# Performance work log

Hardware: AMD Instinct MI355X
Metric: run time of the kernel (lower is better)

## Reference

```python
import jax, jax.numpy as jnp
import numpy as np

B, T, C, H = 1, 4096, 512, 8
HS = C // H  # head size = 64
ROPE_BASE = 10000.0


def setup_inputs() -> dict:
    key = jax.random.key(0)
    k1, k2, k3 = jax.random.split(key, 3)
    x = jax.random.normal(k1, (B, T, C), dtype=jnp.float32)
    W_attn = jax.random.normal(k2, (3 * C, C), dtype=jnp.float32) * 0.02
    W_proj = jax.random.normal(k3, (C, C), dtype=jnp.float32) * 0.02
    # RoPE cache: (T, HS//2, 2) = (cos, sin) per position/frequency
    pos = jnp.arange(T, dtype=jnp.float32)
    inv_freq = 1.0 / (ROPE_BASE ** (jnp.arange(0, HS, 2, dtype=jnp.float32) / HS))
    ang = pos[:, None] * inv_freq[None, :]  # (T, HS//2)
    rope = jnp.stack([jnp.cos(ang), jnp.sin(ang)], axis=-1)
    # causal mask (1,1,T,T), True = attend
    mask = jnp.tril(jnp.ones((T, T), dtype=bool))[None, None]
    return {"x": x, "rope": rope, "mask": mask, "W_attn": W_attn, "W_proj": W_proj}


def apply_rope(x, rope):
    # x: (B, T, H, hs); rope: (>=T, hs//2, 2)
    b, t, h, d = x.shape
    xs = x.reshape(b, t, h, d // 2, 2)
    rc = rope[:t].reshape(1, t, 1, d // 2, 2)
    real = xs[..., 0] * rc[..., 0] - xs[..., 1] * rc[..., 1]
    imag = xs[..., 1] * rc[..., 0] + xs[..., 0] * rc[..., 1]
    return jnp.stack([real, imag], axis=-1).reshape(b, t, h, d)


def reference(x, rope, mask, W_attn, W_proj):
    b, t, c = x.shape
    qkv = x @ W_attn.T  # (B,T,3C)
    q, k, v = jnp.split(qkv, 3, axis=2)
    q = q.reshape(b, t, H, HS)
    k = k.reshape(b, t, H, HS)
    v = v.reshape(b, t, H, HS)
    q = apply_rope(q, rope)
    k = apply_rope(k, rope)
    # (B,H,T,hs)
    q = q.transpose(0, 2, 1, 3)
    k = k.transpose(0, 2, 1, 3)
    v = v.transpose(0, 2, 1, 3)
    scores = jnp.einsum('bhqd,bhkd->bhqk', q, k) * (1.0 / np.sqrt(HS).astype(np.float32))
    scores = jnp.where(mask, scores, -jnp.inf)
    att = jax.nn.softmax(scores, axis=-1)
    y = jnp.einsum('bhqk,bhkd->bhqd', att, v)
    y = y.transpose(0, 2, 1, 3).reshape(b, t, c)
    return y @ W_proj.T
```

## Files before the change

### kernel.cpp

```cpp
#include <hip/hip_runtime.h>

#define T_ 4096
#define C_ 512
#define H_ 8
#define HS_ 64

typedef __attribute__((ext_vector_type(8))) short s16x8;
typedef __attribute__((ext_vector_type(4))) float f32x4;
typedef unsigned int u32;

__device__ __forceinline__ float bf2f(short u) {
    union { float f; unsigned int i; } v;
    v.i = ((unsigned int)(unsigned short)u) << 16;
    return v.f;
}
__device__ __forceinline__ short f2bf(float f) {
    union { float f; unsigned int i; } v;
    v.f = f;
    unsigned int r = (v.i + 0x7FFFu + ((v.i >> 16) & 1u)) >> 16;
    return (short)r;
}

__device__ __forceinline__ void gload_lds16(const short* g, short* l) {
    __builtin_amdgcn_global_load_lds((const __attribute__((address_space(1))) u32*)g,
                                     (__attribute__((address_space(3))) u32*)l,
                                     16, 0, 0);
}

__global__ void cvt3_kernel(const float* __restrict__ x, const float* __restrict__ wa,
                            const float* __restrict__ wp,
                            short* __restrict__ xb, short* __restrict__ wab,
                            short* __restrict__ wpb) {
    int b = blockIdx.x, tid = threadIdx.x;
    const float* src; short* dst; int i;
    if (b < 2048)      { src = x;  dst = xb;  i = b * 256 + tid; }
    else if (b < 2816) { src = wa; dst = wab; i = (b - 2048) * 256 + tid; }
    else               { src = wp; dst = wpb; i = (b - 2816) * 256 + tid; }
    float4 v = ((const float4*)src)[i];
    short4 o;
    o.x = f2bf(v.x); o.y = f2bf(v.y); o.z = f2bf(v.z); o.w = f2bf(v.w);
    ((short4*)dst)[i] = o;
}

template <int BM, int BN, int OUT_BF16>
__global__ __launch_bounds__(256) void gemm_bt(const short* __restrict__ A,
                                               const short* __restrict__ B,
                                               void* __restrict__ Cv,
                                               int M, int N, int K) {
    __shared__ __align__(16) short As[2][BM][64];
    __shared__ __align__(16) short Bs[2][BN][64];
    constexpr int WM = BM / 2, WN = BN / 2;
    constexpr int MR = WM / 16, NR = WN / 16;
    int bn = blockIdx.x, bm = blockIdx.y;
    int tid = threadIdx.x;
    int lane = tid & 63, w = tid >> 6;
    int wr = w >> 1, wc = w & 1;
    int lr = lane & 15, lg = lane >> 4;

    f32x4 acc[MR][NR];
#pragma unroll
    for (int m = 0; m < MR; ++m)
#pragma unroll
        for (int n = 0; n < NR; ++n) acc[m][n] = f32x4{0.f, 0.f, 0.f, 0.f};

    const short* Ab = A + (size_t)bm * BM * K;
    const short* Bb = B + (size_t)bn * BN * K;

    auto stage = [&](int k0, int b) {
#pragma unroll
        for (int i = 0; i < BM / 32; ++i) {
            int c = i * 256 + tid;
            int row = c >> 3, cb = (c & 7) ^ (row & 7);
            gload_lds16(Ab + (size_t)row * K + k0 + cb * 8, &As[b][0][0] + c * 8);
        }
#pragma unroll
        for (int i = 0; i < BN / 32; ++i) {
            int c = i * 256 + tid;
            int row = c >> 3, cb = (c & 7) ^ (row & 7);
            gload_lds16(Bb + (size_t)row * K + k0 + cb * 8, &Bs[b][0][0] + c * 8);
        }
    };
    auto compute = [&](int b) {
#pragma unroll
        for (int kk = 0; kk < 2; ++kk) {
            s16x8 af[MR], bf[NR];
#pragma unroll
            for (int m = 0; m < MR; ++m) {
                int row = wr * WM + m * 16 + lr;
                af[m] = *(const s16x8*)&As[b][row][(((kk * 4 + lg) ^ (row & 7)) << 3)];
            }
#pragma unroll
            for (int n = 0; n < NR; ++n) {
                int row = wc * WN + n * 16 + lr;
                bf[n] = *(const s16x8*)&Bs[b][row][(((kk * 4 + lg) ^ (row & 7)) << 3)];
            }
#pragma unroll
            for (int m = 0; m < MR; ++m)
#pragma unroll
                for (int n = 0; n < NR; ++n)
                    acc[m][n] = __builtin_amdgcn_mfma_f32_16x16x32_bf16(af[m], bf[n], acc[m][n], 0, 0, 0);
        }
    };

    stage(0, 0);
    __syncthreads();
    int nt = K / 64;
    for (int t = 0; t < nt; ++t) {
        int b = t & 1;
        if (t + 1 < nt) stage((t + 1) * 64, b ^ 1);
        compute(b);
        __syncthreads();
    }

#pragma unroll
    for (int m = 0; m < MR; ++m) {
        int row = bm * BM + wr * WM + m * 16 + lg * 4;
#pragma unroll
        for (int n = 0; n < NR; ++n) {
            int col = bn * BN + wc * WN + n * 16 + lr;
#pragma unroll
            for (int i = 0; i < 4; ++i) {
                size_t idx = (size_t)(row + i) * N + col;
                if (OUT_BF16) ((short*)Cv)[idx] = f2bf(acc[m][n][i]);
                else          ((float*)Cv)[idx] = acc[m][n][i];
            }
        }
    }
}

__global__ __launch_bounds__(256) void prep_kernel(const short* __restrict__ qkv,
                                                   const float* __restrict__ rope,
                                                   short* __restrict__ q,
                                                   short* __restrict__ k,
                                                   short* __restrict__ vt) {
    __shared__ short tile[64][72];
    int bt = blockIdx.x, h = blockIdx.y;
    int tid = threadIdx.x;
    const float QS = 0.18033688011112042f;

#pragma unroll
    for (int r = 0; r < 2; ++r) {
        int idx = r * 256 + tid;
        int tt = idx >> 3, c8 = idx & 7;
        int t = bt * 64 + tt;
        const short* row = qkv + (size_t)t * (3 * C_) + h * 64 + c8 * 8;
        s16x8 qv = *(const s16x8*)row;
        s16x8 kv = *(const s16x8*)(row + C_);
        float4 rc0 = *(const float4*)(rope + t * 64 + c8 * 8);
        float4 rc1 = *(const float4*)(rope + t * 64 + c8 * 8 + 4);
        float cs[4] = {rc0.x, rc0.z, rc1.x, rc1.z};
        float sn[4] = {rc0.y, rc0.w, rc1.y, rc1.w};
        s16x8 qo, ko;
#pragma unroll
        for (int p = 0; p < 4; ++p) {
            float qe = bf2f(qv[2 * p]), qd = bf2f(qv[2 * p + 1]);
            float ke = bf2f(kv[2 * p]), kd = bf2f(kv[2 * p + 1]);
            qo[2 * p]     = f2bf((qe * cs[p] - qd * sn[p]) * QS);
            qo[2 * p + 1] = f2bf((qd * cs[p] + qe * sn[p]) * QS);
            ko[2 * p]     = f2bf(ke * cs[p] - kd * sn[p]);
            ko[2 * p + 1] = f2bf(kd * cs[p] + ke * sn[p]);
        }
        size_t o = ((size_t)h * T_ + t) * HS_ + c8 * 8;
        *(s16x8*)(q + o) = qo;
        *(s16x8*)(k + o) = ko;
    }

#pragma unroll
    for (int r = 0; r < 2; ++r) {
        int idx = r * 256 + tid;
        int tt = idx >> 3, c8 = idx & 7;
        *(s16x8*)&tile[tt][c8 * 8] =
            *(const s16x8*)(qkv + (size_t)(bt * 64 + tt) * (3 * C_) + 2 * C_ + h * 64 + c8 * 8);
    }
    __syncthreads();
#pragma unroll
    for (int r = 0; r < 2; ++r) {
        int idx = r * 256 + tid;
        int dd = idx & 63, tg = idx >> 6;
        s16x8 o;
#pragma unroll
        for (int j = 0; j < 8; ++j) o[j] = tile[tg * 8 + j][dd];
        *(s16x8*)(vt + ((size_t)h * HS_ + dd) * T_ + bt * 64 + tg * 8) = o;
    }
}

__global__ __launch_bounds__(256) void attn_kernel(const short* __restrict__ q,
                                                   const short* __restrict__ k,
                                                   const short* __restrict__ vt,
                                                   short* __restrict__ ypart,
                                                   float* __restrict__ lpart) {
    __shared__ __align__(16) short Ks[2][64][64];
    __shared__ __align__(16) short Vs[2][64][64];
    __shared__ __align__(16) short P[4][16][64];
    int bx = blockIdx.x;
    int h = bx & 7;
    int u = bx >> 3;
    int qb = 0, j = u;
    for (int qq = 31; qq >= 0; --qq) {
        int ncq = (qq + 4) >> 2;
        if (j < ncq) { qb = qq; break; }
        j -= ncq;
    }
    int ncq = (qb + 4) >> 2;
    int tiles = 2 * qb + 2;
    int bas = tiles / ncq, rr = tiles % ncq;
    int t0 = j * bas + (j < rr ? j : rr);
    int t1 = t0 + bas + (j < rr ? 1 : 0);

    int tid = threadIdx.x;
    int w = tid >> 6, lane = tid & 63;
    int lr = lane & 15, lg = lane >> 4, x7 = lane & 7;
    int qrow0 = qb * 128 + w * 32;
    const float MC = 12.0f;

    const short* qp = q + ((size_t)h * T_ + qrow0 + lr) * HS_ + lg * 8;
    s16x8 aq0 = *(const s16x8*)qp;
    s16x8 aq1 = *(const s16x8*)(qp + 32);
    s16x8 aq2 = *(const s16x8*)(qp + 16 * HS_);
    s16x8 aq3 = *(const s16x8*)(qp + 16 * HS_ + 32);

    s16x8 bones;
#pragma unroll
    for (int jj = 0; jj < 8; ++jj) bones[jj] = (short)0x3F80;

    f32x4 yA[4], yB[4];
#pragma unroll
    for (int n = 0; n < 4; ++n) { yA[n] = f32x4{0.f,0.f,0.f,0.f}; yB[n] = f32x4{0.f,0.f,0.f,0.f}; }
    f32x4 lAa = f32x4{0.f,0.f,0.f,0.f}, lBa = f32x4{0.f,0.f,0.f,0.f};

    const short* kH = k + (size_t)h * T_ * HS_;
    const short* vH = vt + (size_t)h * HS_ * T_;

    auto stage = [&](short* Kb, short* Vb, int t) {
#pragma unroll
        for (int r = 0; r < 2; ++r) {
            int c = r * 256 + tid;
            int row = c >> 3;
            int cb = (c & 7) ^ (row & 7);
            gload_lds16(kH + (size_t)(t * 64 + row) * HS_ + cb * 8, Kb + c * 8);
            gload_lds16(vH + (size_t)row * T_ + t * 64 + cb * 8, Vb + c * 8);
        }
    };

    short* Pw = &P[w][0][0];

    auto body = [&](int t, const short* Kb, const short* Vb) {
        f32x4 sA[4], sB[4];
#pragma unroll
        for (int c4 = 0; c4 < 4; ++c4) {
            int krow = c4 * 16 + lr;
            const short* kp = Kb + krow * 64;
            s16x8 k0 = *(const s16x8*)(kp + ((lg ^ x7) << 3));
            s16x8 k1 = *(const s16x8*)(kp + (((lg + 4) ^ x7) << 3));
            f32x4 s = f32x4{0.f,0.f,0.f,0.f};
            s = __builtin_amdgcn_mfma_f32_16x16x32_bf16(aq0, k0, s, 0, 0, 0);
            sA[c4] = __builtin_amdgcn_mfma_f32_16x16x32_bf16(aq1, k1, s, 0, 0, 0);
            f32x4 s2 = f32x4{0.f,0.f,0.f,0.f};
            s2 = __builtin_amdgcn_mfma_f32_16x16x32_bf16(aq2, k0, s2, 0, 0, 0);
            sB[c4] = __builtin_amdgcn_mfma_f32_16x16x32_bf16(aq3, k1, s2, 0, 0, 0);
        }
        if (t * 64 + 63 > qrow0) {
#pragma unroll
            for (int c4 = 0; c4 < 4; ++c4) {
                int kcol = t * 64 + c4 * 16 + lr;
#pragma unroll
                for (int i = 0; i < 4; ++i)
                    if (kcol > qrow0 + lg * 4 + i) sA[c4][i] = -1e30f;
            }
        }
        if (t * 64 + 63 > qrow0 + 16) {
#pragma unroll
            for (int c4 = 0; c4 < 4; ++c4) {
                int kcol = t * 64 + c4 * 16 + lr;
#pragma unroll
                for (int i = 0; i < 4; ++i)
                    if (kcol > qrow0 + 16 + lg * 4 + i) sB[c4][i] = -1e30f;
            }
        }
        s16x8 vf[8];
#pragma unroll
        for (int n = 0; n < 4; ++n) {
            int vrow = n * 16 + lr;
            const short* vrp = Vb + vrow * 64;
            vf[2 * n]     = *(const s16x8*)(vrp + ((lg ^ (vrow & 7)) << 3));
            vf[2 * n + 1] = *(const s16x8*)(vrp + (((lg + 4) ^ (vrow & 7)) << 3));
        }
#pragma unroll
        for (int c4 = 0; c4 < 4; ++c4)
#pragma unroll
            for (int i = 0; i < 4; ++i) {
                int row = lg * 4 + i;
                int off = row * 64 + (((c4 * 2 + (lr >> 3)) ^ (row & 7)) << 3) + (lr & 7);
                Pw[off] = f2bf(exp2f(sA[c4][i] - MC));
            }
        s16x8 ap0 = *(const s16x8*)&Pw[lr * 64 + ((lg ^ x7) << 3)];
        s16x8 ap1 = *(const s16x8*)&Pw[lr * 64 + (((lg + 4) ^ x7) << 3)];
        lAa = __builtin_amdgcn_mfma_f32_16x16x32_bf16(ap0, bones, lAa, 0, 0, 0);
        lAa = __builtin_amdgcn_mfma_f32_16x16x32_bf16(ap1, bones, lAa, 0, 0, 0);
#pragma unroll
        for (int n = 0; n < 4; ++n) {
            yA[n] = __builtin_amdgcn_mfma_f32_16x16x32_bf16(ap0, vf[2 * n], yA[n], 0, 0, 0);
            yA[n] = __builtin_amdgcn_mfma_f32_16x16x32_bf16(ap1, vf[2 * n + 1], yA[n], 0, 0, 0);
        }
#pragma unroll
        for (int c4 = 0; c4 < 4; ++c4)
#pragma unroll
            for (int i = 0; i < 4; ++i) {
                int row = lg * 4 + i;
                int off = row * 64 + (((c4 * 2 + (lr >> 3)) ^ (row & 7)) << 3) + (lr & 7);
                Pw[off] = f2bf(exp2f(sB[c4][i] - MC));
            }
        s16x8 bp0 = *(const s16x8*)&Pw[lr * 64 + ((lg ^ x7) << 3)];
        s16x8 bp1 = *(const s16x8*)&Pw[lr * 64 + (((lg + 4) ^ x7) << 3)];
        lBa = __builtin_amdgcn_mfma_f32_16x16x32_bf16(bp0, bones, lBa, 0, 0, 0);
        lBa = __builtin_amdgcn_mfma_f32_16x16x32_bf16(bp1, bones, lBa, 0, 0, 0);
#pragma unroll
        for (int n = 0; n < 4; ++n) {
            yB[n] = __builtin_amdgcn_mfma_f32_16x16x32_bf16(bp0, vf[2 * n], yB[n], 0, 0, 0);
            yB[n] = __builtin_amdgcn_mfma_f32_16x16x32_bf16(bp1, vf[2 * n + 1], yB[n], 0, 0, 0);
        }
    };

    stage(&Ks[0][0][0], &Vs[0][0][0], t0);
    __syncthreads();
    int t = t0;
    for (;;) {
        bool m1 = (t + 1 < t1);
        if (m1) stage(&Ks[1][0][0], &Vs[1][0][0], t + 1);
        body(t, &Ks[0][0][0], &Vs[0][0][0]);
        __syncthreads();
        ++t;
        if (!m1) break;
        bool m2 = (t + 1 < t1);
        if (m2) stage(&Ks[0][0][0], &Vs[0][0][0], t + 1);
        body(t, &Ks[1][0][0], &Vs[1][0][0]);
        __syncthreads();
        ++t;
        if (!m2) break;
    }

    short* yp = ypart + (((size_t)j * H_ + h) * T_ + qrow0) * HS_;
#pragma unroll
    for (int n = 0; n < 4; ++n)
#pragma unroll
        for (int i = 0; i < 4; ++i) {
            yp[(size_t)(lg * 4 + i) * HS_ + n * 16 + lr]      = f2bf(yA[n][i]);
            yp[(size_t)(16 + lg * 4 + i) * HS_ + n * 16 + lr] = f2bf(yB[n][i]);
        }
    if (lr == 0) {
#pragma unroll
        for (int i = 0; i < 4; ++i) {
            size_t r = ((size_t)j * H_ + h) * T_ + qrow0;
            lpart[r + lg * 4 + i]      = lAa[i];
            lpart[r + 16 + lg * 4 + i] = lBa[i];
        }
    }
}

__global__ void combine_kernel(const short* __restrict__ ypart,
                               const float* __restrict__ lpart,
                               short* __restrict__ y) {
    int g = blockIdx.x * 256 + threadIdx.x;
    int c8 = (g & 7) * 8;
    int row = (g >> 3) & 4095;
    int h = g >> 15;
    int nc = ((row >> 7) + 4) >> 2;
    float L = 0.f;
    float acc[8] = {0.f, 0.f, 0.f, 0.f, 0.f, 0.f, 0.f, 0.f};
    for (int c = 0; c < nc; ++c) {
        size_t base = ((size_t)c * H_ + h) * T_ + row;
        L += lpart[base];
        s16x8 yv = *(const s16x8*)(ypart + base * HS_ + c8);
#pragma unroll
        for (int jj = 0; jj < 8; ++jj) acc[jj] += bf2f(yv[jj]);
    }
    float inv = 1.f / L;
    s16x8 o;
#pragma unroll
    for (int jj = 0; jj < 8; ++jj) o[jj] = f2bf(acc[jj] * inv);
    *(s16x8*)(y + (size_t)row * C_ + h * 64 + c8) = o;
}

extern "C" void kernel_launch(void* const* d_in, const int* in_sizes, int n_in,
                              void* d_out, int out_size, void* d_ws, size_t ws_size,
                              hipStream_t stream) {
    const float* x    = (const float*)d_in[0];
    const float* rope = (const float*)d_in[1];
    const float* Wa   = (const float*)d_in[3];
    const float* Wp   = (const float*)d_in[4];
    float* out = (float*)d_out;

    short* ws   = (short*)d_ws;
    short* xb   = ws;
    short* wab  = xb + 2097152;
    short* wpb  = wab + 786432;
    short* qkvb = wpb + 262144;
    short* qws  = qkvb + 6291456;
    short* kws  = qws + 2097152;
    short* vtws = kws + 2097152;
    short* yws  = vtws + 2097152;
    short* ypart = yws + 2097152;
    float* lpart = (float*)(ypart + 16777216);

    cvt3_kernel<<<3072, 256, 0, stream>>>(x, Wa, Wp, xb, wab, wpb);

    gemm_bt<128, 64, 1><<<dim3(24, 32), 256, 0, stream>>>(xb, wab, qkvb, 4096, 1536, 512);

    prep_kernel<<<dim3(64, 8), 256, 0, stream>>>(qkvb, rope, qws, kws, vtws);

    attn_kernel<<<1152, 256, 0, stream>>>(qws, kws, vtws, ypart, lpart);
    combine_kernel<<<1024, 256, 0, stream>>>(ypart, lpart, yws);

    gemm_bt<64, 64, 0><<<dim3(8, 64), 256, 0, stream>>>(yws, wpb, out, 4096, 512, 512);
}
```

Baseline: 181.4 us.

## Fuse RoPE and V transpose into QKV GEMM epilogue; tune attention inner loop

Replaces the separate QKV GEMM plus prep kernel with a single GEMM whose epilogue applies RoPE and the Q scale through lane shuffles, and writes V transposed via an LDS tile. This removes the round trip of the bf16 qkv buffer and one launch. The attention kernel also raises wave priority around its MFMA blocks, uses the hardware exp2 builtin, and truncates P to bf16 instead of rounding. Truncation adds a small bias to the probabilities, and the epilogue now does scalar 2-byte scattered stores for Q and K.

After: 169.4 us. 1.07x faster.

```diff
diff --git a/kernel.cpp b/kernel.cpp
--- a/kernel.cpp
+++ b/kernel.cpp
@@ -8,6 +8,12 @@
 typedef __attribute__((ext_vector_type(8))) short s16x8;
 typedef __attribute__((ext_vector_type(4))) float f32x4;
 typedef unsigned int u32;
+
+#if __has_builtin(__builtin_amdgcn_exp2f)
+#define EXP2(x) __builtin_amdgcn_exp2f(x)
+#else
+#define EXP2(x) exp2f(x)
+#endif
 
 __device__ __forceinline__ float bf2f(short u) {
     union { float f; unsigned int i; } v;
@@ -19,6 +25,9 @@
     v.f = f;
     unsigned int r = (v.i + 0x7FFFu + ((v.i >> 16) & 1u)) >> 16;
     return (short)r;
+}
+__device__ __forceinline__ short bftrunc(float f) {
+    return (short)(__float_as_uint(f) >> 16);
 }
 
 __device__ __forceinline__ void gload_lds16(const short* g, short* l) {
@@ -40,6 +49,123 @@
     short4 o;
     o.x = f2bf(v.x); o.y = f2bf(v.y); o.z = f2bf(v.z); o.w = f2bf(v.w);
     ((short4*)dst)[i] = o;
+}
+
+__global__ __launch_bounds__(256) void gemm_qkv(const short* __restrict__ A,
+                                                const short* __restrict__ B,
+                                                const float* __restrict__ rope,
+                                                short* __restrict__ q,
+                                                short* __restrict__ k,
+                                                short* __restrict__ vt) {
+    constexpr int BM = 128, BN = 64, K = 512;
+    __shared__ __align__(16) short As[2][BM][64];
+    __shared__ __align__(16) short Bs[2][BN][64];
+    constexpr int WM = BM / 2, WN = BN / 2;
+    constexpr int MR = WM / 16, NR = WN / 16;
+    int bn = blockIdx.x, bm = blockIdx.y;
+    int tid = threadIdx.x;
+    int lane = tid & 63, w = tid >> 6;
+    int wr = w >> 1, wc = w & 1;
+    int lr = lane & 15, lg = lane >> 4;
+    const float QS = 0.18033688011112042f;
+
+    f32x4 acc[MR][NR];
+#pragma unroll
+    for (int m = 0; m < MR; ++m)
+#pragma unroll
+        for (int n = 0; n < NR; ++n) acc[m][n] = f32x4{0.f, 0.f, 0.f, 0.f};
+
+    const short* Ab = A + (size_t)bm * BM * K;
+    const short* Bb = B + (size_t)bn * BN * K;
+
+    auto stage = [&](int k0, int b) {
+#pragma unroll
+        for (int i = 0; i < BM / 32; ++i) {
+            int c = i * 256 + tid;
+            int row = c >> 3, cb = (c & 7) ^ (row & 7);
+            gload_lds16(Ab + (size_t)row * K + k0 + cb * 8, &As[b][0][0] + c * 8);
+        }
+#pragma unroll
+        for (int i = 0; i < BN / 32; ++i) {
+            int c = i * 256 + tid;
+            int row = c >> 3, cb = (c & 7) ^ (row & 7);
+            gload_lds16(Bb + (size_t)row * K + k0 + cb * 8, &Bs[b][0][0] + c * 8);
+        }
+    };
+    auto compute = [&](int b) {
+#pragma unroll
+        for (int kk = 0; kk < 2; ++kk) {
+            s16x8 af[MR], bf[NR];
+#pragma unroll
+            for (int m = 0; m < MR; ++m) {
+                int row = wr * WM + m * 16 + lr;
+                af[m] = *(const s16x8*)&As[b][row][(((kk * 4 + lg) ^ (row & 7)) << 3)];
+            }
+#pragma unroll
+            for (int n = 0; n < NR; ++n) {
+                int row = wc * WN + n * 16 + lr;
+                bf[n] = *(const s16x8*)&Bs[b][row][(((kk * 4 + lg) ^ (row & 7)) << 3)];
+            }
+#pragma unroll
+            for (int m = 0; m < MR; ++m)
+#pragma unroll
+                for (int n = 0; n < NR; ++n)
+                    acc[m][n] = __builtin_amdgcn_mfma_f32_16x16x32_bf16(af[m], bf[n], acc[m][n], 0, 0, 0);
+        }
+    };
+
+    stage(0, 0);
+    __syncthreads();
+    constexpr int nt = K / 64;
+    for (int t = 0; t < nt; ++t) {
+        int b = t & 1;
+        if (t + 1 < nt) stage((t + 1) * 64, b ^ 1);
+        compute(b);
+        __syncthreads();
+    }
+
+    int mode = bn >> 3, h = bn & 7;
+    if (mode < 2) {
+        short* dst = mode ? k : q;
+        float scl = mode ? 1.0f : QS;
+#pragma unroll
+        for (int m = 0; m < MR; ++m)
+#pragma unroll
+            for (int n = 0; n < NR; ++n)
+#pragma unroll
+                for (int i = 0; i < 4; ++i) {
+                    int t = bm * BM + wr * WM + m * 16 + lg * 4 + i;
+                    int d = wc * WN + n * 16 + lr;
+                    float v = acc[m][n][i];
+                    float o = __shfl_xor(v, 1);
+                    float2 cs = *(const float2*)(rope + t * 64 + (d & ~1));
+                    float out = v * cs.x + ((lr & 1) ? o * cs.y : -o * cs.y);
+                    dst[((size_t)h * T_ + t) * HS_ + d] = f2bf(out * scl);
+                }
+    } else {
+        short* tile = &As[0][0][0];
+#pragma unroll
+        for (int m = 0; m < MR; ++m)
+#pragma unroll
+            for (int n = 0; n < NR; ++n)
+#pragma unroll
+                for (int i = 0; i < 4; ++i) {
+                    int tl = wr * WM + m * 16 + lg * 4 + i;
+                    int d = wc * WN + n * 16 + lr;
+                    tile[d * 136 + tl] = f2bf(acc[m][n][i]);
+                }
+        __syncthreads();
+#pragma unroll
+        for (int it = 0; it < 2; ++it) {
+            int idx = it * 256 + tid;
+            int r = idx >> 3, c16 = idx & 7;
+            s16x8 a = *(const s16x8*)&tile[r * 136 + c16 * 16];
+            s16x8 b = *(const s16x8*)&tile[r * 136 + c16 * 16 + 8];
+            short* vp = vt + ((size_t)h * HS_ + r) * T_ + bm * BM + c16 * 16;
+            *(s16x8*)vp = a;
+            *(s16x8*)(vp + 8) = b;
+        }
+    }
 }
 
 template <int BM, int BN, int OUT_BF16>
@@ -125,62 +251,6 @@
                 else          ((float*)Cv)[idx] = acc[m][n][i];
             }
         }
-    }
-}
-
-__global__ __launch_bounds__(256) void prep_kernel(const short* __restrict__ qkv,
-                                                   const float* __restrict__ rope,
-                                                   short* __restrict__ q,
-                                                   short* __restrict__ k,
-                                                   short* __restrict__ vt) {
-    __shared__ short tile[64][72];
-    int bt = blockIdx.x, h = blockIdx.y;
-    int tid = threadIdx.x;
-    const float QS = 0.18033688011112042f;
-
-#pragma unroll
-    for (int r = 0; r < 2; ++r) {
-        int idx = r * 256 + tid;
-        int tt = idx >> 3, c8 = idx & 7;
-        int t = bt * 64 + tt;
-        const short* row = qkv + (size_t)t * (3 * C_) + h * 64 + c8 * 8;
-        s16x8 qv = *(const s16x8*)row;
-        s16x8 kv = *(const s16x8*)(row + C_);
-        float4 rc0 = *(const float4*)(rope + t * 64 + c8 * 8);
-        float4 rc1 = *(const float4*)(rope + t * 64 + c8 * 8 + 4);
-        float cs[4] = {rc0.x, rc0.z, rc1.x, rc1.z};
-        float sn[4] = {rc0.y, rc0.w, rc1.y, rc1.w};
-        s16x8 qo, ko;
-#pragma unroll
-        for (int p = 0; p < 4; ++p) {
-            float qe = bf2f(qv[2 * p]), qd = bf2f(qv[2 * p + 1]);
-            float ke = bf2f(kv[2 * p]), kd = bf2f(kv[2 * p + 1]);
-            qo[2 * p]     = f2bf((qe * cs[p] - qd * sn[p]) * QS);
-            qo[2 * p + 1] = f2bf((qd * cs[p] + qe * sn[p]) * QS);
-            ko[2 * p]     = f2bf(ke * cs[p] - kd * sn[p]);
-            ko[2 * p + 1] = f2bf(kd * cs[p] + ke * sn[p]);
-        }
-        size_t o = ((size_t)h * T_ + t) * HS_ + c8 * 8;
-        *(s16x8*)(q + o) = qo;
-        *(s16x8*)(k + o) = ko;
-    }
-
-#pragma unroll
-    for (int r = 0; r < 2; ++r) {
-        int idx = r * 256 + tid;
-        int tt = idx >> 3, c8 = idx & 7;
-        *(s16x8*)&tile[tt][c8 * 8] =
-            *(const s16x8*)(qkv + (size_t)(bt * 64 + tt) * (3 * C_) + 2 * C_ + h * 64 + c8 * 8);
-    }
-    __syncthreads();
-#pragma unroll
-    for (int r = 0; r < 2; ++r) {
-        int idx = r * 256 + tid;
-        int dd = idx & 63, tg = idx >> 6;
-        s16x8 o;
-#pragma unroll
-        for (int j = 0; j < 8; ++j) o[j] = tile[tg * 8 + j][dd];
-        *(s16x8*)(vt + ((size_t)h * HS_ + dd) * T_ + bt * 64 + tg * 8) = o;
     }
 }
 
@@ -246,6 +316,7 @@
 
     auto body = [&](int t, const short* Kb, const short* Vb) {
         f32x4 sA[4], sB[4];
+        __builtin_amdgcn_s_setprio(1);
 #pragma unroll
         for (int c4 = 0; c4 < 4; ++c4) {
             int krow = c4 * 16 + lr;
@@ -259,6 +330,7 @@
             s2 = __builtin_amdgcn_mfma_f32_16x16x32_bf16(aq2, k0, s2, 0, 0, 0);
             sB[c4] = __builtin_amdgcn_mfma_f32_16x16x32_bf16(aq3, k1, s2, 0, 0, 0);
         }
+        __builtin_amdgcn_s_setprio(0);
         if (t * 64 + 63 > qrow0) {
 #pragma unroll
             for (int c4 = 0; c4 < 4; ++c4) {
@@ -291,10 +363,11 @@
             for (int i = 0; i < 4; ++i) {
                 int row = lg * 4 + i;
                 int off = row * 64 + (((c4 * 2 + (lr >> 3)) ^ (row & 7)) << 3) + (lr & 7);
-                Pw[off] = f2bf(exp2f(sA[c4][i] - MC));
+                Pw[off] = bftrunc(EXP2(sA[c4][i] - MC));
             }
         s16x8 ap0 = *(const s16x8*)&Pw[lr * 64 + ((lg ^ x7) << 3)];
         s16x8 ap1 = *(const s16x8*)&Pw[lr * 64 + (((lg + 4) ^ x7) << 3)];
+        __builtin_amdgcn_s_setprio(1);
         lAa = __builtin_amdgcn_mfma_f32_16x16x32_bf16(ap0, bones, lAa, 0, 0, 0);
         lAa = __builtin_amdgcn_mfma_f32_16x16x32_bf16(ap1, bones, lAa, 0, 0, 0);
 #pragma unroll
@@ -302,16 +375,18 @@
             yA[n] = __builtin_amdgcn_mfma_f32_16x16x32_bf16(ap0, vf[2 * n], yA[n], 0, 0, 0);
             yA[n] = __builtin_amdgcn_mfma_f32_16x16x32_bf16(ap1, vf[2 * n + 1], yA[n], 0, 0, 0);
         }
+        __builtin_amdgcn_s_setprio(0);
 #pragma unroll
         for (int c4 = 0; c4 < 4; ++c4)
 #pragma unroll
             for (int i = 0; i < 4; ++i) {
                 int row = lg * 4 + i;
                 int off = row * 64 + (((c4 * 2 + (lr >> 3)) ^ (row & 7)) << 3) + (lr & 7);
-                Pw[off] = f2bf(exp2f(sB[c4][i] - MC));
+                Pw[off] = bftrunc(EXP2(sB[c4][i] - MC));
             }
         s16x8 bp0 = *(const s16x8*)&Pw[lr * 64 + ((lg ^ x7) << 3)];
         s16x8 bp1 = *(const s16x8*)&Pw[lr * 64 + (((lg + 4) ^ x7) << 3)];
+        __builtin_amdgcn_s_setprio(1);
         lBa = __builtin_amdgcn_mfma_f32_16x16x32_bf16(bp0, bones, lBa, 0, 0, 0);
         lBa = __builtin_amdgcn_mfma_f32_16x16x32_bf16(bp1, bones, lBa, 0, 0, 0);
 #pragma unroll
@@ -319,6 +394,7 @@
             yB[n] = __builtin_amdgcn_mfma_f32_16x16x32_bf16(bp0, vf[2 * n], yB[n], 0, 0, 0);
             yB[n] = __builtin_amdgcn_mfma_f32_16x16x32_bf16(bp1, vf[2 * n + 1], yB[n], 0, 0, 0);
         }
+        __builtin_amdgcn_s_setprio(0);
     };
 
     stage(&Ks[0][0][0], &Vs[0][0][0], t0);
@@ -394,8 +470,7 @@
     short* xb   = ws;
     short* wab  = xb + 2097152;
     short* wpb  = wab + 786432;
-    short* qkvb = wpb + 262144;
-    short* qws  = qkvb + 6291456;
+    short* qws  = wpb + 262144;
     short* kws  = qws + 2097152;
     short* vtws = kws + 2097152;
     short* yws  = vtws + 2097152;
@@ -404,9 +479,7 @@
 
     cvt3_kernel<<<3072, 256, 0, stream>>>(x, Wa, Wp, xb, wab, wpb);
 
-    gemm_bt<128, 64, 1><<<dim3(24, 32), 256, 0, stream>>>(xb, wab, qkvb, 4096, 1536, 512);
-
-    prep_kernel<<<dim3(64, 8), 256, 0, stream>>>(qkvb, rope, qws, kws, vtws);
+    gemm_qkv<<<dim3(24, 32), 256, 0, stream>>>(xb, wab, rope, qws, kws, vtws);
 
     attn_kernel<<<1152, 256, 0, stream>>>(qws, kws, vtws, ypart, lpart);
     combine_kernel<<<1024, 256, 0, stream>>>(ypart, lpart, yws);
```
